# Kernel optimization log

Measured on AMD Instinct MI355X. Metric: run time of the kernel, lower is better.

## Reference

```python
import jax, jax.numpy as jnp
import numpy as np

N, P, D, FDIM, TFEAT = 65536, 6, 256, 8, 16
RAW_DIM = 4 + TFEAT  # 20
IN_DIM = 3 + FDIM + 3 + 3  # xyz + frame embedding + rigid xyz + viewdir = 17


def setup_inputs() -> dict:
    key = jax.random.key(0)
    ks = jax.random.split(key, 16)
    inp = {
        "tpts": jax.random.normal(ks[0], (N, P, 3), jnp.float32),
        "bigpts": jax.random.normal(ks[1], (N, P, 3), jnp.float32),
        "viewdir": jax.random.normal(ks[2], (N, P, 3), jnp.float32),
        "dists": jax.random.uniform(ks[3], (N,), jnp.float32),
        "part_dist": jax.random.uniform(ks[4], (1, N, P), jnp.float32),
        "frame_dim": jax.random.normal(ks[5], (FDIM,), jnp.float32),
        "W1": jax.random.normal(ks[6], (P, IN_DIM, D), jnp.float32) / np.sqrt(IN_DIM),
        "b1": jax.random.normal(ks[7], (P, D), jnp.float32) * 0.01,
        "W2": jax.random.normal(ks[8], (P, D, D), jnp.float32) / np.sqrt(D),
        "b2": jax.random.normal(ks[9], (P, D), jnp.float32) * 0.01,
        "W3": jax.random.normal(ks[10], (P, D, RAW_DIM), jnp.float32) / np.sqrt(D),
        "b3": jax.random.normal(ks[11], (P, RAW_DIM), jnp.float32) * 0.01,
        "Wocc": jax.random.normal(ks[12], (P, D, 1), jnp.float32) / np.sqrt(D),
        "bocc": jax.random.normal(ks[13], (P, 1), jnp.float32) * 0.01,
        "tflag": jax.random.randint(ks[14], (N, P), 0, 2).astype(bool),
    }
    return inp


def _part_mlps(tpts, bigpts, viewdir, frame_dim, W1, b1, W2, b2, W3, b3, Wocc, bocc):
    # Run all P part networks on all N points (batched per-part GEMMs).
    n = tpts.shape[0]
    frame = jnp.broadcast_to(frame_dim, (n, P, FDIM))
    x = jnp.concatenate([tpts, frame, bigpts, viewdir], axis=-1)  # (N,P,17)
    h = jax.nn.relu(jnp.einsum('npi,pid->npd', x, W1) + b1)
    h = jax.nn.relu(jnp.einsum('npd,pde->npe', h, W2) + b2)
    raw_p = jnp.einsum('npd,pdr->npr', h, W3) + b3               # (N,P,20)
    occ_p = jax.nn.sigmoid(jnp.einsum('npd,pdo->npo', h, Wocc) + bocc)  # (N,P,1)
    return raw_p, occ_p


def reference(tpts, bigpts, viewdir, dists, part_dist, frame_dim,
              W1, b1, W2, b2, W3, b3, Wocc, bocc, tflag):
    raw_p, occ_p = _part_mlps(tpts, bigpts, viewdir, frame_dim,
                              W1, b1, W2, b2, W3, b3, Wocc, bocc)
    # scatter-back equivalent: unflagged (point, part) slots stay zero
    flag = tflag[..., None].astype(raw_p.dtype)  # (N,P,1)
    raws = raw_p * flag                           # (N,P,20)
    occs = occ_p * flag                           # (N,P,1)
    # cfg.aggr == 'mean'
    raw = raws.mean(axis=1)                       # (N,20)
    occ = occs.mean(axis=1)                       # (N,1)
    tocc = occs[..., 0]                           # (N,P)
    return jnp.concatenate([raw, occ, tocc], axis=-1)  # (N, 20+1+P)
```

## Files before the change

kernel.cpp:

```cpp
#include <hip/hip_runtime.h>
#include <hip/hip_bf16.h>

using bf16 = __hip_bfloat16;
using uint = unsigned int;
typedef __bf16 bf16x8 __attribute__((ext_vector_type(8)));
typedef __bf16 bf16x4v __attribute__((ext_vector_type(4)));
typedef float f32x4 __attribute__((ext_vector_type(4)));

#define MFMA16(a, b, c) __builtin_amdgcn_mfma_f32_16x16x32_bf16((a), (b), (c), 0, 0, 0)


__global__ void prep_kernel(const float* __restrict__ W1, const float* __restrict__ b1,
                            const float* __restrict__ W2, const float* __restrict__ W3,
                            const float* __restrict__ Wocc, __bf16* __restrict__ ws) {
  const int t = blockIdx.x * 256 + threadIdx.x;
  if (t < 49152) {
    const int p = t >> 13, r = t & 8191, n = r >> 5, c = r & 31;
    const float* src = W2 + p * 65536 + c * 8 * 256 + n;
    bf16x8 v;
#pragma unroll
    for (int j = 0; j < 8; ++j) v[j] = (__bf16)src[j * 256];
    *reinterpret_cast<bf16x8*>(&ws[49152 + p * 65536 + n * 256 + c * 8]) = v;
  } else if (t < 55296) {
    const int u = t - 49152;
    const int p = u >> 10, r = u & 1023, n = r >> 2, c = r & 3;
    bf16x8 v;
#pragma unroll
    for (int j = 0; j < 8; ++j) {
      const int k = c * 8 + j;
      float x = 0.f;
      if (k < 17) {
        const int ko = (k < 8) ? k + 3 : ((k < 11) ? k - 8 : k);
        x = W1[p * 4352 + ko * 256 + n];
      } else if (k == 17) {
        x = b1[p * 256 + n];
      }
      v[j] = (__bf16)x;
    }
    *reinterpret_cast<bf16x8*>(&ws[p * 8192 + n * 32 + c * 8]) = v;
  } else if (t < 61440) {
    const int u = t - 55296;
    const int p = u >> 10, r = u & 1023, row = r >> 5, c = r & 31;
    bf16x8 v;
#pragma unroll
    for (int j = 0; j < 8; ++j) {
      const int k = c * 8 + j;
      float x = 0.f;
      if (row < 20)       x = W3[p * 5120 + k * 20 + row];
      else if (row == 20) x = Wocc[p * 256 + k];
      v[j] = (__bf16)x;
    }
    *reinterpret_cast<bf16x8*>(&ws[442368 + p * 8192 + row * 256 + c * 8]) = v;
  }
}

__global__ __launch_bounds__(256, 2) void tpose_main(
    const float* __restrict__ tpts, const float* __restrict__ bigpts,
    const float* __restrict__ viewdir, const float* __restrict__ frame,
    const float* __restrict__ b2g, const float* __restrict__ b3g,
    const float* __restrict__ boccg, const int* __restrict__ tflag,
    const __bf16* __restrict__ ws, float* __restrict__ out) {
  const __bf16* __restrict__ W1t = ws;
  const __bf16* __restrict__ W2t = ws + 49152;
  const __bf16* __restrict__ W3t = ws + 442368;

  __shared__ __align__(16) __bf16 Xf[128 * 40];
  __shared__ __align__(16) __bf16 Hf[128 * 256];
  __shared__ float Ts[128 * 6];

  const int tid = threadIdx.x;
  const int w = tid >> 6;
  const int lane = tid & 63;
  const int lq = lane >> 4;
  const int ln = lane & 15;
  const int e = ln & 7;
  const int n0 = blockIdx.x * 128;

  if (tid < 128) {
    bf16x8 f8;
#pragma unroll
    for (int j = 0; j < 8; ++j) f8[j] = (__bf16)frame[j];
    *reinterpret_cast<bf16x8*>(&Xf[tid * 40]) = f8;
    bf16x8 z = {};
    z[1] = (__bf16)1.0f;
    *reinterpret_cast<bf16x8*>(&Xf[tid * 40 + 16]) = z;
    bf16x8 z2 = {};
    *reinterpret_cast<bf16x8*>(&Xf[tid * 40 + 24]) = z2;
  }

  const int role = tid & 3;
  const float* __restrict__ dynsrc =
      (role == 0) ? tpts : (role == 1) ? bigpts : viewdir;

  float pre[2][3];
  float flv[2];
#pragma unroll
  for (int pass = 0; pass < 2; ++pass) {
    const int pt = (tid >> 2) + pass * 64;
    const int base3 = (n0 + pt) * 18;
#pragma unroll
    for (int i = 0; i < 3; ++i) pre[pass][i] = dynsrc[base3 + i];
  }
#pragma unroll
  for (int s = 0; s < 2; ++s)
    flv[s] = (tflag[(n0 + w * 32 + s * 16 + ln) * 6] != 0) ? 1.f : 0.f;

  float psum0[2][4] = {{0.f, 0.f, 0.f, 0.f}, {0.f, 0.f, 0.f, 0.f}};
  float psum1[2][4] = {{0.f, 0.f, 0.f, 0.f}, {0.f, 0.f, 0.f, 0.f}};

  for (int p = 0; p < 6; ++p) {
    if (role < 3) {
#pragma unroll
      for (int pass = 0; pass < 2; ++pass) {
        const int pt = (tid >> 2) + pass * 64;
#pragma unroll
        for (int i = 0; i < 3; ++i)
          Xf[pt * 40 + 8 + role * 3 + i] = (__bf16)pre[pass][i];
      }
    }

    const int pn = (p < 5) ? p + 1 : 5;
    float fln[2];
#pragma unroll
    for (int pass = 0; pass < 2; ++pass) {
      const int pt = (tid >> 2) + pass * 64;
      const int base3 = ((n0 + pt) * 6 + pn) * 3;
#pragma unroll
      for (int i = 0; i < 3; ++i) pre[pass][i] = dynsrc[base3 + i];
    }
#pragma unroll
    for (int s = 0; s < 2; ++s)
      fln[s] = (tflag[(n0 + w * 32 + s * 16 + ln) * 6 + pn] != 0) ? 1.f : 0.f;

    bf16x8 aw[4];
#pragma unroll
    for (int mt = 0; mt < 4; ++mt)
      aw[mt] = *reinterpret_cast<const bf16x8*>(
          &W1t[p * 8192 + (w * 64 + mt * 16 + ln) * 32 + lq * 8]);

    __syncthreads();

    f32x4 acc[4][8];
#pragma unroll
    for (int mt = 0; mt < 4; ++mt)
#pragma unroll
      for (int nt = 0; nt < 8; ++nt) acc[mt][nt] = f32x4{0.f, 0.f, 0.f, 0.f};
#pragma unroll
    for (int nt = 0; nt < 8; ++nt) {
      const bf16x8 xb =
          *reinterpret_cast<const bf16x8*>(&Xf[(nt * 16 + ln) * 40 + lq * 8]);
#pragma unroll
      for (int mt = 0; mt < 4; ++mt) acc[mt][nt] = MFMA16(aw[mt], xb, acc[mt][nt]);
    }
#pragma unroll
    for (int mt = 0; mt < 4; ++mt) {
      const int c = w * 8 + mt * 2 + (lq >> 1);
      const int off = ((c ^ e) << 3) + (lq & 1) * 4;
#pragma unroll
      for (int nt = 0; nt < 8; ++nt) {
        bf16x4v hv;
#pragma unroll
        for (int r = 0; r < 4; ++r) hv[r] = (__bf16)fmaxf(acc[mt][nt][r], 0.f);
        *reinterpret_cast<bf16x4v*>(&Hf[(nt * 16 + ln) * 256 + off]) = hv;
      }
    }

    __syncthreads();

    {
      f32x4 b2v[4];
#pragma unroll
      for (int mt = 0; mt < 4; ++mt)
        b2v[mt] = *reinterpret_cast<const f32x4*>(
            &b2g[p * 256 + w * 64 + mt * 16 + lq * 4]);
#pragma unroll
      for (int mt = 0; mt < 4; ++mt)
#pragma unroll
        for (int nt = 0; nt < 8; ++nt) acc[mt][nt] = b2v[mt];
    }
    const __bf16* __restrict__ w2p = W2t + p * 65536 + (w * 64 + ln) * 256 + lq * 8;
    {
      bf16x8 a2[4];
#pragma unroll
      for (int mt = 0; mt < 4; ++mt)
        a2[mt] = *reinterpret_cast<const bf16x8*>(w2p + mt * 4096);
#pragma unroll
      for (int kk = 0; kk < 8; ++kk) {
        bf16x8 a2n[4];
        if (kk < 7) {
#pragma unroll
          for (int mt = 0; mt < 4; ++mt)
            a2n[mt] = *reinterpret_cast<const bf16x8*>(
                w2p + mt * 4096 + (kk + 1) * 32);
        }
#pragma unroll
        for (int nt = 0; nt < 8; ++nt) {
          const bf16x8 hb = *reinterpret_cast<const bf16x8*>(
              &Hf[(nt * 16 + ln) * 256 + (((kk * 4 + lq) ^ e) << 3)]);
#pragma unroll
          for (int mt = 0; mt < 4; ++mt) acc[mt][nt] = MFMA16(a2[mt], hb, acc[mt][nt]);
        }
#pragma unroll
        for (int mt = 0; mt < 4; ++mt) a2[mt] = a2n[mt];
      }
    }

    __syncthreads();

#pragma unroll
    for (int mt = 0; mt < 4; ++mt) {
      const int c = w * 8 + mt * 2 + (lq >> 1);
      const int off = ((c ^ e) << 3) + (lq & 1) * 4;
#pragma unroll
      for (int nt = 0; nt < 8; ++nt) {
        bf16x4v hv;
#pragma unroll
        for (int r = 0; r < 4; ++r) hv[r] = (__bf16)fmaxf(acc[mt][nt][r], 0.f);
        *reinterpret_cast<bf16x4v*>(&Hf[(nt * 16 + ln) * 256 + off]) = hv;
      }
    }

    __syncthreads();

    f32x4 acc3[2][2];
    {
      float b3v[2][4];
#pragma unroll
      for (int mt = 0; mt < 2; ++mt)
#pragma unroll
        for (int r = 0; r < 4; ++r) {
          const int d = mt * 16 + lq * 4 + r;
          float v = 0.f;
          if (d < 20)       v = b3g[p * 20 + d];
          else if (d == 20) v = boccg[p];
          b3v[mt][r] = v;
        }
#pragma unroll
      for (int mt = 0; mt < 2; ++mt)
#pragma unroll
        for (int s = 0; s < 2; ++s)
#pragma unroll
          for (int r = 0; r < 4; ++r) acc3[mt][s][r] = b3v[mt][r];
    }
    const __bf16* __restrict__ w3p = W3t + p * 8192 + ln * 256 + lq * 8;
#pragma unroll
    for (int kk = 0; kk < 8; ++kk) {
      bf16x8 a3[2];
#pragma unroll
      for (int mt = 0; mt < 2; ++mt)
        a3[mt] = *reinterpret_cast<const bf16x8*>(w3p + mt * 4096 + kk * 32);
#pragma unroll
      for (int s = 0; s < 2; ++s) {
        const bf16x8 hb = *reinterpret_cast<const bf16x8*>(
            &Hf[(w * 32 + s * 16 + ln) * 256 + (((kk * 4 + lq) ^ e) << 3)]);
#pragma unroll
        for (int mt = 0; mt < 2; ++mt) acc3[mt][s] = MFMA16(a3[mt], hb, acc3[mt][s]);
      }
    }

#pragma unroll
    for (int s = 0; s < 2; ++s) {
      const int ptl = w * 32 + s * 16 + ln;
#pragma unroll
      for (int r = 0; r < 4; ++r) psum0[s][r] += flv[s] * acc3[0][s][r];
      if (lq == 0) {
#pragma unroll
        for (int r = 0; r < 4; ++r) psum1[s][r] += flv[s] * acc3[1][s][r];
      } else if (lq == 1) {
        const float occ = 1.f / (1.f + __expf(-acc3[1][s][0]));
        Ts[ptl * 6 + p] = flv[s] * occ;
        psum1[s][0] += flv[s] * occ;
      }
    }

    flv[0] = fln[0];
    flv[1] = fln[1];
  }

  __syncthreads();

  float* __restrict__ Sg = reinterpret_cast<float*>(Hf);
  const float inv6 = 1.f / 6.f;
#pragma unroll
  for (int s = 0; s < 2; ++s) {
    const int ptl = w * 32 + s * 16 + ln;
#pragma unroll
    for (int r = 0; r < 4; ++r) Sg[ptl * 27 + lq * 4 + r] = psum0[s][r] * inv6;
    if (lq == 0) {
#pragma unroll
      for (int r = 0; r < 4; ++r) Sg[ptl * 27 + 16 + r] = psum1[s][r] * inv6;
    } else if (lq == 1) {
      Sg[ptl * 27 + 20] = psum1[s][0] * inv6;
#pragma unroll
      for (int i = 0; i < 6; ++i) Sg[ptl * 27 + 21 + i] = Ts[ptl * 6 + i];
    }
  }

  __syncthreads();

  {
    const f32x4* __restrict__ src4 = reinterpret_cast<const f32x4*>(Sg);
    f32x4* __restrict__ dst4 = reinterpret_cast<f32x4*>(out + n0 * 27);
    for (int i = tid; i < 864; i += 256) dst4[i] = src4[i];
  }
}

extern "C" void kernel_launch(void* const* d_in, const int* in_sizes, int n_in,
                              void* d_out, int out_size, void* d_ws, size_t ws_size,
                              hipStream_t stream) {
  const float* tpts    = (const float*)d_in[0];
  const float* bigpts  = (const float*)d_in[1];
  const float* viewdir = (const float*)d_in[2];
  const float* frame   = (const float*)d_in[5];
  const float* W1      = (const float*)d_in[6];
  const float* b1      = (const float*)d_in[7];
  const float* W2      = (const float*)d_in[8];
  const float* b2      = (const float*)d_in[9];
  const float* W3      = (const float*)d_in[10];
  const float* b3      = (const float*)d_in[11];
  const float* Wocc    = (const float*)d_in[12];
  const float* bocc    = (const float*)d_in[13];
  const int*   tflag   = (const int*)d_in[14];
  __bf16* ws  = (__bf16*)d_ws;
  float*  out = (float*)d_out;

  prep_kernel<<<240, 256, 0, stream>>>(W1, b1, W2, W3, Wocc, ws);
  tpose_main<<<512, 256, 0, stream>>>(tpts, bigpts, viewdir, frame, b2, b3,
                                      bocc, tflag, ws, out);
}
```

Baseline: 199.6 us.

## Halve block to 64 points with two waves covering 128 features each

The main kernel now runs 128 threads per block on 64 points, launching twice as many blocks with half the shared memory each. Each wave now computes a 128-feature by 64-point tile instead of 64 by 128, and the input staging is reassigned so two threads share each point. The goal is better load balance and higher occupancy across CUs. In exchange, every block streams the full W2 weights for only half as many points, which doubles weight traffic per point. The register prefetch of the next W2 fragment is also dropped, so those loads are no longer overlapped with the MFMAs.

```diff
diff --git a/kernel.cpp b/kernel.cpp
--- a/kernel.cpp
+++ b/kernel.cpp
@@ -54,7 +54,7 @@
   }
 }
 
-__global__ __launch_bounds__(256, 2) void tpose_main(
+__global__ __launch_bounds__(128, 2) void tpose_main(
     const float* __restrict__ tpts, const float* __restrict__ bigpts,
     const float* __restrict__ viewdir, const float* __restrict__ frame,
     const float* __restrict__ b2g, const float* __restrict__ b3g,
@@ -64,9 +64,9 @@
   const __bf16* __restrict__ W2t = ws + 49152;
   const __bf16* __restrict__ W3t = ws + 442368;
 
-  __shared__ __align__(16) __bf16 Xf[128 * 40];
-  __shared__ __align__(16) __bf16 Hf[128 * 256];
-  __shared__ float Ts[128 * 6];
+  __shared__ __align__(16) __bf16 Xf[64 * 40];
+  __shared__ __align__(16) __bf16 Hf[64 * 256];
+  __shared__ float Ts[64 * 6];
 
   const int tid = threadIdx.x;
   const int w = tid >> 6;
@@ -74,9 +74,9 @@
   const int lq = lane >> 4;
   const int ln = lane & 15;
   const int e = ln & 7;
-  const int n0 = blockIdx.x * 128;
-
-  if (tid < 128) {
+  const int n0 = blockIdx.x * 64;
+
+  if (tid < 64) {
     bf16x8 f8;
 #pragma unroll
     for (int j = 0; j < 8; ++j) f8[j] = (__bf16)frame[j];
@@ -88,18 +88,20 @@
     *reinterpret_cast<bf16x8*>(&Xf[tid * 40 + 24]) = z2;
   }
 
-  const int role = tid & 3;
-  const float* __restrict__ dynsrc =
-      (role == 0) ? tpts : (role == 1) ? bigpts : viewdir;
-
-  float pre[2][3];
+  const int role = tid & 1;
+  const int apt = tid >> 1;
+  const float* __restrict__ s1 = role ? viewdir : tpts;
+
+  float pre[6];
   float flv[2];
-#pragma unroll
-  for (int pass = 0; pass < 2; ++pass) {
-    const int pt = (tid >> 2) + pass * 64;
-    const int base3 = (n0 + pt) * 18;
-#pragma unroll
-    for (int i = 0; i < 3; ++i) pre[pass][i] = dynsrc[base3 + i];
+  {
+    const int base3 = (n0 + apt) * 18;
+#pragma unroll
+    for (int i = 0; i < 3; ++i) pre[i] = s1[base3 + i];
+    if (role == 0) {
+#pragma unroll
+      for (int i = 0; i < 3; ++i) pre[3 + i] = bigpts[base3 + i];
+    }
   }
 #pragma unroll
   for (int s = 0; s < 2; ++s)
@@ -109,55 +111,57 @@
   float psum1[2][4] = {{0.f, 0.f, 0.f, 0.f}, {0.f, 0.f, 0.f, 0.f}};
 
   for (int p = 0; p < 6; ++p) {
-    if (role < 3) {
-#pragma unroll
-      for (int pass = 0; pass < 2; ++pass) {
-        const int pt = (tid >> 2) + pass * 64;
-#pragma unroll
-        for (int i = 0; i < 3; ++i)
-          Xf[pt * 40 + 8 + role * 3 + i] = (__bf16)pre[pass][i];
-      }
+    if (role == 0) {
+#pragma unroll
+      for (int i = 0; i < 3; ++i) Xf[apt * 40 + 8 + i] = (__bf16)pre[i];
+#pragma unroll
+      for (int i = 0; i < 3; ++i) Xf[apt * 40 + 11 + i] = (__bf16)pre[3 + i];
+    } else {
+#pragma unroll
+      for (int i = 0; i < 3; ++i) Xf[apt * 40 + 14 + i] = (__bf16)pre[i];
     }
 
     const int pn = (p < 5) ? p + 1 : 5;
     float fln[2];
-#pragma unroll
-    for (int pass = 0; pass < 2; ++pass) {
-      const int pt = (tid >> 2) + pass * 64;
-      const int base3 = ((n0 + pt) * 6 + pn) * 3;
-#pragma unroll
-      for (int i = 0; i < 3; ++i) pre[pass][i] = dynsrc[base3 + i];
+    {
+      const int base3 = ((n0 + apt) * 6 + pn) * 3;
+#pragma unroll
+      for (int i = 0; i < 3; ++i) pre[i] = s1[base3 + i];
+      if (role == 0) {
+#pragma unroll
+        for (int i = 0; i < 3; ++i) pre[3 + i] = bigpts[base3 + i];
+      }
     }
 #pragma unroll
     for (int s = 0; s < 2; ++s)
       fln[s] = (tflag[(n0 + w * 32 + s * 16 + ln) * 6 + pn] != 0) ? 1.f : 0.f;
 
-    bf16x8 aw[4];
-#pragma unroll
-    for (int mt = 0; mt < 4; ++mt)
+    bf16x8 aw[8];
+#pragma unroll
+    for (int mt = 0; mt < 8; ++mt)
       aw[mt] = *reinterpret_cast<const bf16x8*>(
-          &W1t[p * 8192 + (w * 64 + mt * 16 + ln) * 32 + lq * 8]);
+          &W1t[p * 8192 + (w * 128 + mt * 16 + ln) * 32 + lq * 8]);
 
     __syncthreads();
 
-    f32x4 acc[4][8];
-#pragma unroll
-    for (int mt = 0; mt < 4; ++mt)
-#pragma unroll
-      for (int nt = 0; nt < 8; ++nt) acc[mt][nt] = f32x4{0.f, 0.f, 0.f, 0.f};
-#pragma unroll
-    for (int nt = 0; nt < 8; ++nt) {
+    f32x4 acc[8][4];
+#pragma unroll
+    for (int mt = 0; mt < 8; ++mt)
+#pragma unroll
+      for (int nt = 0; nt < 4; ++nt) acc[mt][nt] = f32x4{0.f, 0.f, 0.f, 0.f};
+#pragma unroll
+    for (int nt = 0; nt < 4; ++nt) {
       const bf16x8 xb =
           *reinterpret_cast<const bf16x8*>(&Xf[(nt * 16 + ln) * 40 + lq * 8]);
 #pragma unroll
-      for (int mt = 0; mt < 4; ++mt) acc[mt][nt] = MFMA16(aw[mt], xb, acc[mt][nt]);
-    }
-#pragma unroll
-    for (int mt = 0; mt < 4; ++mt) {
-      const int c = w * 8 + mt * 2 + (lq >> 1);
+      for (int mt = 0; mt < 8; ++mt) acc[mt][nt] = MFMA16(aw[mt], xb, acc[mt][nt]);
+    }
+#pragma unroll
+    for (int mt = 0; mt < 8; ++mt) {
+      const int c = w * 16 + mt * 2 + (lq >> 1);
       const int off = ((c ^ e) << 3) + (lq & 1) * 4;
 #pragma unroll
-      for (int nt = 0; nt < 8; ++nt) {
+      for (int nt = 0; nt < 4; ++nt) {
         bf16x4v hv;
 #pragma unroll
         for (int r = 0; r < 4; ++r) hv[r] = (__bf16)fmaxf(acc[mt][nt][r], 0.f);
@@ -168,51 +172,40 @@
     __syncthreads();
 
     {
-      f32x4 b2v[4];
-#pragma unroll
-      for (int mt = 0; mt < 4; ++mt)
+      f32x4 b2v[8];
+#pragma unroll
+      for (int mt = 0; mt < 8; ++mt)
         b2v[mt] = *reinterpret_cast<const f32x4*>(
-            &b2g[p * 256 + w * 64 + mt * 16 + lq * 4]);
-#pragma unroll
-      for (int mt = 0; mt < 4; ++mt)
-#pragma unroll
-        for (int nt = 0; nt < 8; ++nt) acc[mt][nt] = b2v[mt];
-    }
-    const __bf16* __restrict__ w2p = W2t + p * 65536 + (w * 64 + ln) * 256 + lq * 8;
-    {
-      bf16x8 a2[4];
-#pragma unroll
-      for (int mt = 0; mt < 4; ++mt)
-        a2[mt] = *reinterpret_cast<const bf16x8*>(w2p + mt * 4096);
-#pragma unroll
-      for (int kk = 0; kk < 8; ++kk) {
-        bf16x8 a2n[4];
-        if (kk < 7) {
-#pragma unroll
-          for (int mt = 0; mt < 4; ++mt)
-            a2n[mt] = *reinterpret_cast<const bf16x8*>(
-                w2p + mt * 4096 + (kk + 1) * 32);
-        }
-#pragma unroll
-        for (int nt = 0; nt < 8; ++nt) {
-          const bf16x8 hb = *reinterpret_cast<const bf16x8*>(
-              &Hf[(nt * 16 + ln) * 256 + (((kk * 4 + lq) ^ e) << 3)]);
-#pragma unroll
-          for (int mt = 0; mt < 4; ++mt) acc[mt][nt] = MFMA16(a2[mt], hb, acc[mt][nt]);
-        }
-#pragma unroll
-        for (int mt = 0; mt < 4; ++mt) a2[mt] = a2n[mt];
+            &b2g[p * 256 + w * 128 + mt * 16 + lq * 4]);
+#pragma unroll
+      for (int mt = 0; mt < 8; ++mt)
+#pragma unroll
+        for (int nt = 0; nt < 4; ++nt) acc[mt][nt] = b2v[mt];
+    }
+    const __bf16* __restrict__ w2p = W2t + p * 65536 + (w * 128 + ln) * 256 + lq * 8;
+#pragma unroll
+    for (int kk = 0; kk < 8; ++kk) {
+      bf16x8 a2[8];
+#pragma unroll
+      for (int mt = 0; mt < 8; ++mt)
+        a2[mt] = *reinterpret_cast<const bf16x8*>(w2p + mt * 4096 + kk * 32);
+#pragma unroll
+      for (int nt = 0; nt < 4; ++nt) {
+        const bf16x8 hb = *reinterpret_cast<const bf16x8*>(
+            &Hf[(nt * 16 + ln) * 256 + (((kk * 4 + lq) ^ e) << 3)]);
+#pragma unroll
+        for (int mt = 0; mt < 8; ++mt) acc[mt][nt] = MFMA16(a2[mt], hb, acc[mt][nt]);
       }
     }
 
     __syncthreads();
 
 #pragma unroll
-    for (int mt = 0; mt < 4; ++mt) {
-      const int c = w * 8 + mt * 2 + (lq >> 1);
+    for (int mt = 0; mt < 8; ++mt) {
+      const int c = w * 16 + mt * 2 + (lq >> 1);
       const int off = ((c ^ e) << 3) + (lq & 1) * 4;
 #pragma unroll
-      for (int nt = 0; nt < 8; ++nt) {
+      for (int nt = 0; nt < 4; ++nt) {
         bf16x4v hv;
 #pragma unroll
         for (int r = 0; r < 4; ++r) hv[r] = (__bf16)fmaxf(acc[mt][nt][r], 0.f);
@@ -301,7 +294,7 @@
   {
     const f32x4* __restrict__ src4 = reinterpret_cast<const f32x4*>(Sg);
     f32x4* __restrict__ dst4 = reinterpret_cast<f32x4*>(out + n0 * 27);
-    for (int i = tid; i < 864; i += 256) dst4[i] = src4[i];
+    for (int i = tid; i < 432; i += 128) dst4[i] = src4[i];
   }
 }
 
@@ -325,6 +318,6 @@
   float*  out = (float*)d_out;
 
   prep_kernel<<<240, 256, 0, stream>>>(W1, b1, W2, W3, Wocc, ws);
-  tpose_main<<<512, 256, 0, stream>>>(tpts, bigpts, viewdir, frame, b2, b3,
-                                      bocc, tflag, ws, out);
+  tpose_main<<<1024, 128, 0, stream>>>(tpts, bigpts, viewdir, frame, b2, b3,
+                                       bocc, tflag, ws, out);
 }
```

After: 273.7 us. 37.1% more time.
